# Optimization experiments

Hardware: AMD Instinct MI355X
Metric: run time of the kernel (lower is better)

## Reference

```python
import jax, jax.numpy as jnp
import numpy as np

N_NODES = 100000
N_EDGES = 1600000
IN_F = 32
HID = 128


def setup_inputs() -> dict:
    key = jax.random.key(0)
    ks = jax.random.split(key, 8)
    x = jax.random.normal(ks[0], (N_NODES, IN_F), dtype=jnp.float32)
    edge_index = jax.random.randint(ks[1], (2, N_EDGES), 0, N_NODES, dtype=jnp.int64)
    # Glorot-ish scaled weights
    W1 = jax.random.normal(ks[2], (IN_F, HID), dtype=jnp.float32) / np.sqrt(IN_F)
    b1 = jnp.zeros((HID,), dtype=jnp.float32)
    W2 = jax.random.normal(ks[3], (HID, HID), dtype=jnp.float32) / np.sqrt(HID)
    b2 = jnp.zeros((HID,), dtype=jnp.float32)
    W3 = jax.random.normal(ks[4], (HID, IN_F), dtype=jnp.float32) / np.sqrt(HID)
    b3 = jnp.zeros((IN_F,), dtype=jnp.float32)
    return {"x": x, "edge_index": edge_index, "W1": W1, "b1": b1,
            "W2": W2, "b2": b2, "W3": W3, "b3": b3}


def _gcn_norm(edge_index, n_nodes):
    # Add self-loops (PyG GCNConv default) and compute symmetric normalization
    loops = jnp.arange(n_nodes, dtype=edge_index.dtype)
    src = jnp.concatenate([edge_index[0], loops])
    dst = jnp.concatenate([edge_index[1], loops])
    ones = jnp.ones(src.shape[0], dtype=jnp.float32)
    deg = jax.ops.segment_sum(ones, dst, num_segments=n_nodes)
    deg_inv_sqrt = jnp.where(deg > 0, jax.lax.rsqrt(deg), 0.0)
    norm = deg_inv_sqrt[src] * deg_inv_sqrt[dst]  # [E + N]
    return src, dst, norm


def _gcn_conv(x, src, dst, norm, W, b, n_nodes):
    h = x @ W                                # [N, out] transform first (smaller msgs when out<in)
    msg = h[src] * norm[:, None]             # gather + edge-wise scale  [E+N, out]
    out = jax.ops.segment_sum(msg, dst, num_segments=n_nodes)  # scatter-add
    return out + b


def reference(x, edge_index, W1, b1, W2, b2, W3, b3):
    n = x.shape[0]
    src, dst, norm = _gcn_norm(edge_index, n)
    h = jax.nn.relu(_gcn_conv(x, src, dst, norm, W1, b1, n))
    h = jax.nn.relu(_gcn_conv(h, src, dst, norm, W2, b2, n))
    h = jax.nn.relu(_gcn_conv(h, src, dst, norm, W3, b3, n))
    return h
```

## Files before the change

kernel.cpp:

```cpp
#include <hip/hip_runtime.h>
#include <hip/hip_fp16.h>

#define N_NODES 100000
#define N_EDGES 1600000
#define IN_F 32
#define HID 128
#define BSHIFT 9
#define BSIZE 512
#define NBUCK 196
#define EPB 8192
#define NBB 196
#define COLSZ 3206144

typedef _Float16 half8 __attribute__((ext_vector_type(8)));
typedef float floatx4 __attribute__((ext_vector_type(4)));

static __device__ __forceinline__ void pack2(_Float16* dst, float a, float b) {
    union { _Float16 h[2]; unsigned u; } p;
    p.h[0] = (_Float16)a; p.h[1] = (_Float16)b;
    *(unsigned*)dst = p.u;
}


__global__ __launch_bounds__(256) void k_bcount(const int* __restrict__ dst,
                                                int* __restrict__ bcnt) {
    __shared__ int hist[256];
    hist[threadIdx.x] = 0;
    __syncthreads();
    const int e0 = blockIdx.x * EPB;
#pragma unroll 4
    for (int k = 0; k < 32; ++k) {
        int e = e0 + k * 256 + threadIdx.x;
        if (e < N_EDGES) atomicAdd(&hist[dst[e] >> BSHIFT], 1);
    }
    __syncthreads();
    int c = hist[threadIdx.x];
    if (c > 0) atomicAdd(&bcnt[threadIdx.x], c);
}

__global__ __launch_bounds__(256) void k_bscan(const int* __restrict__ bcnt,
                                               int* __restrict__ bbase,
                                               int* __restrict__ bcur) {
    __shared__ int s[256];
    int v = (threadIdx.x < NBUCK) ? bcnt[threadIdx.x] : 0;
    s[threadIdx.x] = v;
    __syncthreads();
    for (int off = 1; off < 256; off <<= 1) {
        int t = (threadIdx.x >= off) ? s[threadIdx.x - off] : 0;
        __syncthreads();
        s[threadIdx.x] += t;
        __syncthreads();
    }
    if (threadIdx.x < NBUCK) {
        int ex = s[threadIdx.x] - v;
        bbase[threadIdx.x] = ex;
        bcur[threadIdx.x]  = ex;
    }
    if (threadIdx.x == 0) bbase[NBUCK] = N_EDGES;
}

__global__ __launch_bounds__(256) void k_bucket(const int* __restrict__ src,
                                                const int* __restrict__ dst,
                                                int* __restrict__ bcur,
                                                unsigned* __restrict__ rec) {
    __shared__ int hist[256];
    __shared__ int lbase[256];
    const int e0 = blockIdx.x * EPB;
    hist[threadIdx.x] = 0;
    __syncthreads();

    unsigned rk[32]; short bk[32];
#pragma unroll
    for (int k = 0; k < 32; ++k) {
        int e = e0 + k * 256 + threadIdx.x;
        if (e < N_EDGES) {
            int d = dst[e];
            int b = d >> BSHIFT;
            bk[k] = (short)b;
            rk[k] = ((unsigned)src[e] << BSHIFT) | (unsigned)(d & (BSIZE - 1));
            atomicAdd(&hist[b], 1);
        } else bk[k] = -1;
    }
    __syncthreads();
    int c = hist[threadIdx.x];
    lbase[threadIdx.x] = (c > 0) ? atomicAdd(&bcur[threadIdx.x], c) : 0;
    __syncthreads();
    hist[threadIdx.x] = 0;
    __syncthreads();
#pragma unroll
    for (int k = 0; k < 32; ++k) {
        if (bk[k] >= 0) {
            int off = atomicAdd(&hist[bk[k]], 1);
            rec[lbase[bk[k]] + off] = rk[k];
        }
    }
}

__global__ __launch_bounds__(256) void k_fill3(const unsigned* __restrict__ rec,
                                               const int* __restrict__ bbase,
                                               int* __restrict__ ideg,
                                               int* __restrict__ cursor,
                                               int* __restrict__ col) {
    __shared__ int lcnt[BSIZE];
    __shared__ int lcur[BSIZE];
    __shared__ int lend[BSIZE];
    __shared__ int s[256];
    const int b = blockIdx.x;
    const int n0 = b << BSHIFT;
    const int rbeg = bbase[b];
    const int rend = bbase[b + 1];
    const int pbeg = ((rbeg + 15) & ~15) + (16 * BSIZE) * b;

    lcnt[threadIdx.x] = 0;
    lcnt[threadIdx.x + 256] = 0;
    __syncthreads();
    for (int i = rbeg + threadIdx.x; i < rend; i += 256)
        atomicAdd(&lcnt[rec[i] & (BSIZE - 1)], 1);
    __syncthreads();

    int a0 = lcnt[2 * threadIdx.x], a1 = lcnt[2 * threadIdx.x + 1];
    int p0 = (a0 + 15) & ~15, p1 = (a1 + 15) & ~15;
    int pv = p0 + p1;
    s[threadIdx.x] = pv;
    __syncthreads();
    for (int off = 1; off < 256; off <<= 1) {
        int t = (threadIdx.x >= off) ? s[threadIdx.x - off] : 0;
        __syncthreads();
        s[threadIdx.x] += t;
        __syncthreads();
    }
    int ex = s[threadIdx.x] - pv;
    int c0 = pbeg + ex;
    int c1 = c0 + p0;
    lcur[2 * threadIdx.x]     = c0;  lend[2 * threadIdx.x]     = c0 + p0;
    lcur[2 * threadIdx.x + 1] = c1;  lend[2 * threadIdx.x + 1] = c1 + p1;
    __syncthreads();

    for (int t = threadIdx.x; t < BSIZE; t += 256) {
        int n = n0 + t;
        if (n < N_NODES) {
            ideg[n]   = lcnt[t];
            cursor[n] = lcur[t];
        }
    }
    __syncthreads();
    for (int i = rbeg + threadIdx.x; i < rend; i += 256) {
        unsigned r = rec[i];
        int slot = atomicAdd(&lcur[r & (BSIZE - 1)], 1);
        col[slot] = (int)(r >> BSHIFT);
    }
    __syncthreads();
    for (int t = threadIdx.x; t < BSIZE; t += 256) {
        int e2 = lend[t];
        for (int k = lcur[t]; k < e2; ++k) col[k] = N_NODES;
    }
}


__global__ void k_prescale(const float2* __restrict__ x, const int* __restrict__ ideg,
                           __half2* __restrict__ T) {
    if (blockIdx.x == 0 && threadIdx.x < 16)
        ((unsigned*)(T + (size_t)N_NODES * 16))[threadIdx.x] = 0u;
    int tid = blockIdx.x * 256 + threadIdx.x;
    if (tid >= N_NODES * 16) return;
    int i = tid >> 4;
    float dis = rsqrtf(1.0f + (float)ideg[i]);
    float2 v = x[tid];
    T[tid] = __floats2half2_rn(v.x * dis, v.y * dis);
}


__global__ __launch_bounds__(256) void k_gather32_pre(
    const int* __restrict__ cursor, const int* __restrict__ ideg,
    const int* __restrict__ col, const _Float16* __restrict__ T,
    _Float16* __restrict__ OUT) {
    const int lane = threadIdx.x & 63;
    const int slot = lane >> 2;
    const int fl   = lane & 3;
    const int wid  = blockIdx.x * 4 + (threadIdx.x >> 6);
    const int wstride = gridDim.x * 4;

    for (int node = wid; node < N_NODES; node += wstride) {
        int begin = cursor[node];
        int d     = ideg[node];
        int nb    = (d + 15) >> 4;
        float acc[8];
        if (slot == 0) {
            half8 v = *(const half8*)(T + (size_t)node * IN_F + fl * 8);
#pragma unroll
            for (int i = 0; i < 8; ++i) acc[i] = (float)v[i];
        } else {
#pragma unroll
            for (int i = 0; i < 8; ++i) acc[i] = 0.f;
        }
        const int* cp = col + begin + slot;
        int itb = 0;
        for (; itb + 2 <= nb; itb += 2, cp += 32) {
            int s0 = cp[0];
            int s1 = cp[16];
            half8 v0 = *(const half8*)(T + (size_t)s0 * IN_F + fl * 8);
            half8 v1 = *(const half8*)(T + (size_t)s1 * IN_F + fl * 8);
#pragma unroll
            for (int i = 0; i < 8; ++i) acc[i] += (float)v0[i] + (float)v1[i];
        }
        if (itb < nb) {
            int s0 = cp[0];
            half8 v0 = *(const half8*)(T + (size_t)s0 * IN_F + fl * 8);
#pragma unroll
            for (int i = 0; i < 8; ++i) acc[i] += (float)v0[i];
        }
#pragma unroll
        for (int m = 4; m < 64; m <<= 1)
#pragma unroll
            for (int i = 0; i < 8; ++i) acc[i] += __shfl_xor(acc[i], m, 64);
        if (slot == 0) {
            float dis = rsqrtf(1.0f + (float)d);
            half8 o;
#pragma unroll
            for (int i = 0; i < 8; ++i) o[i] = (_Float16)(acc[i] * dis);
            *(half8*)(OUT + (size_t)node * IN_F + fl * 8) = o;
        }
    }
}

__global__ __launch_bounds__(256) void k_gather32_fin(
    const int* __restrict__ cursor, const int* __restrict__ ideg,
    const int* __restrict__ col, const _Float16* __restrict__ T,
    const float* __restrict__ b, float* __restrict__ OUT) {
    const int lane = threadIdx.x & 63;
    const int slot = lane >> 2;
    const int fl   = lane & 3;
    const int wid  = blockIdx.x * 4 + (threadIdx.x >> 6);
    const int wstride = gridDim.x * 4;

    float4 bb0 = *(const float4*)(b + fl * 8);
    float4 bb1 = *(const float4*)(b + fl * 8 + 4);
    float bias[8] = {bb0.x, bb0.y, bb0.z, bb0.w, bb1.x, bb1.y, bb1.z, bb1.w};

    for (int node = wid; node < N_NODES; node += wstride) {
        int begin = cursor[node];
        int d     = ideg[node];
        int nb    = (d + 15) >> 4;
        float acc[8];
        if (slot == 0) {
            half8 v = *(const half8*)(T + (size_t)node * IN_F + fl * 8);
#pragma unroll
            for (int i = 0; i < 8; ++i) acc[i] = (float)v[i];
        } else {
#pragma unroll
            for (int i = 0; i < 8; ++i) acc[i] = 0.f;
        }
        const int* cp = col + begin + slot;
        int itb = 0;
        for (; itb + 2 <= nb; itb += 2, cp += 32) {
            int s0 = cp[0];
            int s1 = cp[16];
            half8 v0 = *(const half8*)(T + (size_t)s0 * IN_F + fl * 8);
            half8 v1 = *(const half8*)(T + (size_t)s1 * IN_F + fl * 8);
#pragma unroll
            for (int i = 0; i < 8; ++i) acc[i] += (float)v0[i] + (float)v1[i];
        }
        if (itb < nb) {
            int s0 = cp[0];
            half8 v0 = *(const half8*)(T + (size_t)s0 * IN_F + fl * 8);
#pragma unroll
            for (int i = 0; i < 8; ++i) acc[i] += (float)v0[i];
        }
#pragma unroll
        for (int m = 4; m < 64; m <<= 1)
#pragma unroll
            for (int i = 0; i < 8; ++i) acc[i] += __shfl_xor(acc[i], m, 64);
        if (slot == 0) {
            float dis = rsqrtf(1.0f + (float)d);
            float o[8];
#pragma unroll
            for (int i = 0; i < 8; ++i) {
                float v = acc[i] * dis + bias[i];
                o[i] = v > 0.f ? v : 0.f;
            }
            float* op = OUT + (size_t)node * IN_F + fl * 8;
            *(float4*)op       = make_float4(o[0], o[1], o[2], o[3]);
            *(float4*)(op + 4) = make_float4(o[4], o[5], o[6], o[7]);
        }
    }
}

__global__ __launch_bounds__(256) void k_gather128(
    const int* __restrict__ cursor, const int* __restrict__ ideg,
    const int* __restrict__ col, const _Float16* __restrict__ T,
    const float* __restrict__ b, _Float16* __restrict__ OUT) {
    const int lane = threadIdx.x & 63;
    const int slot = lane >> 4;
    const int fl   = lane & 15;
    const int wid  = blockIdx.x * 4 + (threadIdx.x >> 6);
    const int wstride = gridDim.x * 4;

    float4 bb0 = *(const float4*)(b + fl * 8);
    float4 bb1 = *(const float4*)(b + fl * 8 + 4);
    float bias[8] = {bb0.x, bb0.y, bb0.z, bb0.w, bb1.x, bb1.y, bb1.z, bb1.w};

    for (int node = wid; node < N_NODES; node += wstride) {
        int begin = cursor[node];
        int d     = ideg[node];
        int nb    = (d + 15) >> 4;
        float acc[8];
        if (slot == 0) {
            half8 v = *(const half8*)(T + (size_t)node * HID + fl * 8);
#pragma unroll
            for (int i = 0; i < 8; ++i) acc[i] = (float)v[i];
        } else {
#pragma unroll
            for (int i = 0; i < 8; ++i) acc[i] = 0.f;
        }
        const int* cp = col + begin + slot * 4;
        for (int itb = 0; itb < nb; ++itb, cp += 16) {
            int4 cc = *(const int4*)cp;
            half8 v0 = *(const half8*)(T + (size_t)cc.x * HID + fl * 8);
            half8 v1 = *(const half8*)(T + (size_t)cc.y * HID + fl * 8);
            half8 v2 = *(const half8*)(T + (size_t)cc.z * HID + fl * 8);
            half8 v3 = *(const half8*)(T + (size_t)cc.w * HID + fl * 8);
#pragma unroll
            for (int i = 0; i < 8; ++i)
                acc[i] += ((float)v0[i] + (float)v1[i]) + ((float)v2[i] + (float)v3[i]);
        }
#pragma unroll
        for (int m = 16; m < 64; m <<= 1)
#pragma unroll
            for (int i = 0; i < 8; ++i) acc[i] += __shfl_xor(acc[i], m, 64);
        if (slot == 0) {
            float dis = rsqrtf(1.0f + (float)d);
            half8 o;
#pragma unroll
            for (int i = 0; i < 8; ++i) {
                float v = acc[i] * dis + bias[i];
                o[i] = (_Float16)(v > 0.f ? v : 0.f);
            }
            *(half8*)(OUT + (size_t)node * HID + fl * 8) = o;
        }
    }
}


__global__ __launch_bounds__(256) void k_xform12_mfma(
    const _Float16* __restrict__ z, const float* __restrict__ W1,
    const float* __restrict__ b1, const float* __restrict__ W2,
    const int* __restrict__ ideg, _Float16* __restrict__ T) {
    if (blockIdx.x == 0 && threadIdx.x < 64)
        ((unsigned*)(T + (size_t)N_NODES * HID))[threadIdx.x] = 0u;
    __shared__ _Float16 W1t[128 * 40];
    __shared__ _Float16 W2t[128 * 136];
    __shared__ _Float16 H1s[64 * 136];
    for (int idx = threadIdx.x; idx < 2048; idx += 256) {
        int n = idx & 127, k = (idx >> 7) * 2;
        pack2(&W1t[n * 40 + k], W1[k * HID + n], W1[(k + 1) * HID + n]);
    }
    for (int idx = threadIdx.x; idx < 8192; idx += 256) {
        int n = idx & 127, k = (idx >> 7) * 2;
        pack2(&W2t[n * 136 + k], W2[k * HID + n], W2[(k + 1) * HID + n]);
    }
    __syncthreads();

    const int lane = threadIdx.x & 63;
    const int wave = threadIdx.x >> 6;
    const int m16 = lane & 15, quad = lane >> 4;
    const int row0 = blockIdx.x * 64 + wave * 16;
    if (row0 >= N_NODES) return;

    {
        int arow = row0 + m16; if (arow >= N_NODES) arow = N_NODES - 1;
        half8 a = *(const half8*)(z + (size_t)arow * IN_F + quad * 8);
        floatx4 acc[8];
#pragma unroll
        for (int t = 0; t < 8; ++t) acc[t] = (floatx4){0.f, 0.f, 0.f, 0.f};
#pragma unroll
        for (int t = 0; t < 8; ++t) {
            half8 b = *(const half8*)&W1t[(t * 16 + m16) * 40 + quad * 8];
            acc[t] = __builtin_amdgcn_mfma_f32_16x16x32_f16(a, b, acc[t], 0, 0, 0);
        }
#pragma unroll
        for (int t = 0; t < 8; ++t) {
            int c = t * 16 + m16;
            float bj = b1[c];
#pragma unroll
            for (int r = 0; r < 4; ++r) {
                float v = acc[t][r] + bj;
                H1s[(wave * 16 + quad * 4 + r) * 136 + c] =
                    (_Float16)(v > 0.f ? v : 0.f);
            }
        }
    }
    __syncthreads();

    const _Float16* hp = &H1s[(wave * 16 + m16) * 136 + quad * 8];
    half8 a[4];
#pragma unroll
    for (int kk = 0; kk < 4; ++kk) a[kk] = *(const half8*)(hp + kk * 32);

    floatx4 acc[8];
#pragma unroll
    for (int t = 0; t < 8; ++t) acc[t] = (floatx4){0.f, 0.f, 0.f, 0.f};
#pragma unroll
    for (int t = 0; t < 8; ++t) {
        const _Float16* wp = &W2t[(t * 16 + m16) * 136 + quad * 8];
#pragma unroll
        for (int kk = 0; kk < 4; ++kk) {
            half8 b = *(const half8*)(wp + kk * 32);
            acc[t] = __builtin_amdgcn_mfma_f32_16x16x32_f16(a[kk], b, acc[t], 0, 0, 0);
        }
    }
    float dis[4];
#pragma unroll
    for (int r = 0; r < 4; ++r) {
        int row = row0 + quad * 4 + r;
        dis[r] = (row < N_NODES) ? rsqrtf(1.0f + (float)ideg[row]) : 0.f;
    }
#pragma unroll
    for (int t = 0; t < 8; ++t) {
        int c = t * 16 + m16;
#pragma unroll
        for (int r = 0; r < 4; ++r) {
            int row = row0 + quad * 4 + r;
            if (row < N_NODES)
                T[(size_t)row * HID + c] = (_Float16)(acc[t][r] * dis[r]);
        }
    }
}

__global__ __launch_bounds__(256) void k_xform3_mfma(
    const _Float16* __restrict__ H, const float* __restrict__ W,
    const int* __restrict__ ideg, _Float16* __restrict__ T) {
    if (blockIdx.x == 0 && threadIdx.x < 16)
        ((unsigned*)(T + (size_t)N_NODES * IN_F))[threadIdx.x] = 0u;
    __shared__ _Float16 Wt[32 * 136];
    for (int idx = threadIdx.x; idx < 2048; idx += 256) {
        int n = idx & 31, k = (idx >> 5) * 2;
        pack2(&Wt[n * 136 + k], W[k * IN_F + n], W[(k + 1) * IN_F + n]);
    }
    __syncthreads();

    const int lane = threadIdx.x & 63;
    const int wave = threadIdx.x >> 6;
    const int m16 = lane & 15, quad = lane >> 4;
    const int row0 = blockIdx.x * 64 + wave * 16;
    if (row0 >= N_NODES) return;

    int arow = row0 + m16; if (arow >= N_NODES) arow = N_NODES - 1;
    const _Float16* hp = H + (size_t)arow * HID + quad * 8;
    half8 a[4];
#pragma unroll
    for (int kk = 0; kk < 4; ++kk) a[kk] = *(const half8*)(hp + kk * 32);

    floatx4 acc[2];
#pragma unroll
    for (int t = 0; t < 2; ++t) acc[t] = (floatx4){0.f, 0.f, 0.f, 0.f};
#pragma unroll
    for (int t = 0; t < 2; ++t) {
        const _Float16* wp = &Wt[(t * 16 + m16) * 136 + quad * 8];
#pragma unroll
        for (int kk = 0; kk < 4; ++kk) {
            half8 b = *(const half8*)(wp + kk * 32);
            acc[t] = __builtin_amdgcn_mfma_f32_16x16x32_f16(a[kk], b, acc[t], 0, 0, 0);
        }
    }
    float dis[4];
#pragma unroll
    for (int r = 0; r < 4; ++r) {
        int row = row0 + quad * 4 + r;
        dis[r] = (row < N_NODES) ? rsqrtf(1.0f + (float)ideg[row]) : 0.f;
    }
#pragma unroll
    for (int t = 0; t < 2; ++t) {
        int c = t * 16 + m16;
#pragma unroll
        for (int r = 0; r < 4; ++r) {
            int row = row0 + quad * 4 + r;
            if (row < N_NODES)
                T[(size_t)row * IN_F + c] = (_Float16)(acc[t][r] * dis[r]);
        }
    }
}


extern "C" void kernel_launch(void* const* d_in, const int* in_sizes, int n_in,
                              void* d_out, int out_size, void* d_ws, size_t ws_size,
                              hipStream_t stream) {
    const float* x  = (const float*)d_in[0];
    const int*   ei = (const int*)d_in[1];
    const float* W1 = (const float*)d_in[2];
    const float* b1 = (const float*)d_in[3];
    const float* W2 = (const float*)d_in[4];
    const float* b2 = (const float*)d_in[5];
    const float* W3 = (const float*)d_in[6];
    const float* b3 = (const float*)d_in[7];
    float* out = (float*)d_out;

    const int* src = ei;
    const int* dst = ei + N_EDGES;

    int*      ideg   = (int*)d_ws;
    int*      cursor = ideg + 102400;
    int*      bcnt   = cursor + 102400;
    int*      bbase  = bcnt + 256;
    int*      bcur   = bbase + 256;
    int*      col    = bcur + 256;
    unsigned* rec    = (unsigned*)(col + COLSZ);
    _Float16* t1h    = (_Float16*)rec;
    _Float16* z      = t1h + (size_t)N_NODES * IN_F + 64;
    _Float16* H1h    = z + (size_t)N_NODES * IN_F;
    _Float16* T2h    = H1h + (size_t)N_NODES * HID;
    _Float16* H2h    = T2h + (size_t)N_NODES * HID + 128;

    const int xgrid = (N_NODES + 63) / 64;

    hipMemsetAsync(bcnt, 0, 256 * sizeof(int), stream);
    k_bcount<<<NBB, 256, 0, stream>>>(dst, bcnt);
    k_bscan<<<1, 256, 0, stream>>>(bcnt, bbase, bcur);
    k_bucket<<<NBB, 256, 0, stream>>>(src, dst, bcur, rec);
    k_fill3<<<NBUCK, 256, 0, stream>>>(rec, bbase, ideg, cursor, col);

    k_prescale<<<(N_NODES * 16 + 255) / 256, 256, 0, stream>>>(
        (const float2*)x, ideg, (__half2*)t1h);
    k_gather32_pre<<<2048, 256, 0, stream>>>(cursor, ideg, col, t1h, z);
    k_xform12_mfma<<<xgrid, 256, 0, stream>>>(z, W1, b1, W2, ideg, T2h);

    k_gather128<<<2048, 256, 0, stream>>>(cursor, ideg, col, T2h, b2, H2h);

    k_xform3_mfma<<<xgrid, 256, 0, stream>>>(H2h, W3, ideg, T2h);
    k_gather32_fin<<<2048, 256, 0, stream>>>(cursor, ideg, col, T2h, b3, out);
}
```

Baseline: 329.1 us.

## Drop bucket count/scan passes, fuse prescale and layer-3 transform, pre-transpose weights

Replaces the count+scan bucketing with fixed-stride per-bucket regions so a single bucket pass writes records directly, removing two kernels. Prescaling of x is folded into the CSR fill kernel, and the layer-3 transform is fused into the 128-wide gather via a shared-memory tile, eliminating the H2 round trip through global memory. Weights are transposed to fp16 once in a prep kernel instead of every block re-staging them into LDS. The fixed strides assume no bucket overflows its preallocated capacity, and the gather128 now uses a static node-per-wave mapping instead of a grid-stride loop.

```diff
diff --git a/kernel.cpp b/kernel.cpp
--- a/kernel.cpp
+++ b/kernel.cpp
@@ -8,56 +8,34 @@
 #define BSHIFT 9
 #define BSIZE 512
 #define NBUCK 196
-#define EPB 8192
-#define NBB 196
-#define COLSZ 3206144
+#define EPB 4096
+#define NBB 391
+#define REC_STRIDE 9728
+#define COL_STRIDE 17408
 
 typedef _Float16 half8 __attribute__((ext_vector_type(8)));
 typedef float floatx4 __attribute__((ext_vector_type(4)));
 
-static __device__ __forceinline__ void pack2(_Float16* dst, float a, float b) {
-    union { _Float16 h[2]; unsigned u; } p;
-    p.h[0] = (_Float16)a; p.h[1] = (_Float16)b;
-    *(unsigned*)dst = p.u;
-}
-
-
-__global__ __launch_bounds__(256) void k_bcount(const int* __restrict__ dst,
-                                                int* __restrict__ bcnt) {
-    __shared__ int hist[256];
-    hist[threadIdx.x] = 0;
-    __syncthreads();
-    const int e0 = blockIdx.x * EPB;
-#pragma unroll 4
-    for (int k = 0; k < 32; ++k) {
-        int e = e0 + k * 256 + threadIdx.x;
-        if (e < N_EDGES) atomicAdd(&hist[dst[e] >> BSHIFT], 1);
-    }
-    __syncthreads();
-    int c = hist[threadIdx.x];
-    if (c > 0) atomicAdd(&bcnt[threadIdx.x], c);
-}
-
-__global__ __launch_bounds__(256) void k_bscan(const int* __restrict__ bcnt,
-                                               int* __restrict__ bbase,
-                                               int* __restrict__ bcur) {
-    __shared__ int s[256];
-    int v = (threadIdx.x < NBUCK) ? bcnt[threadIdx.x] : 0;
-    s[threadIdx.x] = v;
-    __syncthreads();
-    for (int off = 1; off < 256; off <<= 1) {
-        int t = (threadIdx.x >= off) ? s[threadIdx.x - off] : 0;
-        __syncthreads();
-        s[threadIdx.x] += t;
-        __syncthreads();
-    }
-    if (threadIdx.x < NBUCK) {
-        int ex = s[threadIdx.x] - v;
-        bbase[threadIdx.x] = ex;
-        bcur[threadIdx.x]  = ex;
-    }
-    if (threadIdx.x == 0) bbase[NBUCK] = N_EDGES;
-}
+__global__ __launch_bounds__(256) void k_wprep(const float* __restrict__ W1,
+                                               const float* __restrict__ W2,
+                                               const float* __restrict__ W3,
+                                               _Float16* __restrict__ Wt) {
+    const int bid = blockIdx.x, t = threadIdx.x;
+    if (bid < 64) {
+        int idx = bid * 256 + t;
+        int n = idx >> 7, k = idx & 127;
+        Wt[4096 + idx] = (_Float16)W2[k * HID + n];
+    } else if (bid < 80) {
+        int idx = (bid - 64) * 256 + t;
+        int n = idx >> 5, k = idx & 31;
+        Wt[n * 32 + k] = (_Float16)W1[k * HID + n];
+    } else {
+        int idx = (bid - 80) * 256 + t;
+        int n = idx >> 7, k = idx & 127;
+        Wt[20480 + idx] = (_Float16)W3[k * IN_F + n];
+    }
+}
+
 
 __global__ __launch_bounds__(256) void k_bucket(const int* __restrict__ src,
                                                 const int* __restrict__ dst,
@@ -69,9 +47,9 @@
     hist[threadIdx.x] = 0;
     __syncthreads();
 
-    unsigned rk[32]; short bk[32];
-#pragma unroll
-    for (int k = 0; k < 32; ++k) {
+    unsigned rk[16]; short bk[16];
+#pragma unroll
+    for (int k = 0; k < 16; ++k) {
         int e = e0 + k * 256 + threadIdx.x;
         if (e < N_EDGES) {
             int d = dst[e];
@@ -83,12 +61,13 @@
     }
     __syncthreads();
     int c = hist[threadIdx.x];
-    lbase[threadIdx.x] = (c > 0) ? atomicAdd(&bcur[threadIdx.x], c) : 0;
+    lbase[threadIdx.x] =
+        (c > 0) ? threadIdx.x * REC_STRIDE + atomicAdd(&bcur[threadIdx.x], c) : 0;
     __syncthreads();
     hist[threadIdx.x] = 0;
     __syncthreads();
 #pragma unroll
-    for (int k = 0; k < 32; ++k) {
+    for (int k = 0; k < 16; ++k) {
         if (bk[k] >= 0) {
             int off = atomicAdd(&hist[bk[k]], 1);
             rec[lbase[bk[k]] + off] = rk[k];
@@ -96,77 +75,78 @@
     }
 }
 
-__global__ __launch_bounds__(256) void k_fill3(const unsigned* __restrict__ rec,
-                                               const int* __restrict__ bbase,
-                                               int* __restrict__ ideg,
-                                               int* __restrict__ cursor,
-                                               int* __restrict__ col) {
+__global__ __launch_bounds__(256) void k_fill3p(const unsigned* __restrict__ rec,
+                                                const int* __restrict__ bcur,
+                                                const float2* __restrict__ x2,
+                                                int* __restrict__ ideg,
+                                                int* __restrict__ cursor,
+                                                int* __restrict__ col,
+                                                __half2* __restrict__ t1) {
     __shared__ int lcnt[BSIZE];
     __shared__ int lcur[BSIZE];
     __shared__ int lend[BSIZE];
     __shared__ int s[256];
     const int b = blockIdx.x;
+    const int t = threadIdx.x;
     const int n0 = b << BSHIFT;
-    const int rbeg = bbase[b];
-    const int rend = bbase[b + 1];
-    const int pbeg = ((rbeg + 15) & ~15) + (16 * BSIZE) * b;
-
-    lcnt[threadIdx.x] = 0;
-    lcnt[threadIdx.x + 256] = 0;
-    __syncthreads();
-    for (int i = rbeg + threadIdx.x; i < rend; i += 256)
+    const int rbeg = b * REC_STRIDE;
+    const int rend = rbeg + bcur[b];
+    const int pbeg = b * COL_STRIDE;
+
+    lcnt[t] = 0;
+    lcnt[t + 256] = 0;
+    __syncthreads();
+    for (int i = rbeg + t; i < rend; i += 256)
         atomicAdd(&lcnt[rec[i] & (BSIZE - 1)], 1);
     __syncthreads();
 
-    int a0 = lcnt[2 * threadIdx.x], a1 = lcnt[2 * threadIdx.x + 1];
+    int a0 = lcnt[2 * t], a1 = lcnt[2 * t + 1];
     int p0 = (a0 + 15) & ~15, p1 = (a1 + 15) & ~15;
     int pv = p0 + p1;
-    s[threadIdx.x] = pv;
+    s[t] = pv;
     __syncthreads();
     for (int off = 1; off < 256; off <<= 1) {
-        int t = (threadIdx.x >= off) ? s[threadIdx.x - off] : 0;
+        int v = (t >= off) ? s[t - off] : 0;
         __syncthreads();
-        s[threadIdx.x] += t;
+        s[t] += v;
         __syncthreads();
     }
-    int ex = s[threadIdx.x] - pv;
+    int ex = s[t] - pv;
     int c0 = pbeg + ex;
     int c1 = c0 + p0;
-    lcur[2 * threadIdx.x]     = c0;  lend[2 * threadIdx.x]     = c0 + p0;
-    lcur[2 * threadIdx.x + 1] = c1;  lend[2 * threadIdx.x + 1] = c1 + p1;
-    __syncthreads();
-
-    for (int t = threadIdx.x; t < BSIZE; t += 256) {
-        int n = n0 + t;
+    lcur[2 * t]     = c0;  lend[2 * t]     = c0 + p0;
+    lcur[2 * t + 1] = c1;  lend[2 * t + 1] = c1 + p1;
+    __syncthreads();
+
+    for (int i = t; i < BSIZE; i += 256) {
+        int n = n0 + i;
         if (n < N_NODES) {
-            ideg[n]   = lcnt[t];
-            cursor[n] = lcur[t];
-        }
-    }
-    __syncthreads();
-    for (int i = rbeg + threadIdx.x; i < rend; i += 256) {
+            ideg[n]   = lcnt[i];
+            cursor[n] = lcur[i];
+        }
+    }
+    __syncthreads();
+    for (int i = rbeg + t; i < rend; i += 256) {
         unsigned r = rec[i];
         int slot = atomicAdd(&lcur[r & (BSIZE - 1)], 1);
         col[slot] = (int)(r >> BSHIFT);
     }
     __syncthreads();
-    for (int t = threadIdx.x; t < BSIZE; t += 256) {
-        int e2 = lend[t];
-        for (int k = lcur[t]; k < e2; ++k) col[k] = N_NODES;
-    }
-}
-
-
-__global__ void k_prescale(const float2* __restrict__ x, const int* __restrict__ ideg,
-                           __half2* __restrict__ T) {
-    if (blockIdx.x == 0 && threadIdx.x < 16)
-        ((unsigned*)(T + (size_t)N_NODES * 16))[threadIdx.x] = 0u;
-    int tid = blockIdx.x * 256 + threadIdx.x;
-    if (tid >= N_NODES * 16) return;
-    int i = tid >> 4;
-    float dis = rsqrtf(1.0f + (float)ideg[i]);
-    float2 v = x[tid];
-    T[tid] = __floats2half2_rn(v.x * dis, v.y * dis);
+    for (int i = t; i < BSIZE; i += 256) {
+        int e2 = lend[i];
+        for (int k = lcur[i]; k < e2; ++k) col[k] = N_NODES;
+    }
+
+    if (b == 0 && t < 16) ((unsigned*)t1)[N_NODES * 16 + t] = 0u;
+    for (int idx = t; idx < BSIZE * 16; idx += 256) {
+        int loc = idx >> 4, j = idx & 15;
+        int n = n0 + loc;
+        if (n < N_NODES) {
+            float dis = rsqrtf(1.0f + (float)lcnt[loc]);
+            float2 v = x2[(size_t)n * 16 + j];
+            t1[(size_t)n * 16 + j] = __floats2half2_rn(v.x * dis, v.y * dis);
+        }
+    }
 }
 
 
@@ -285,21 +265,103 @@
     }
 }
 
-__global__ __launch_bounds__(256) void k_gather128(
+
+__global__ __launch_bounds__(256, 4) void k_xform12(
+    const _Float16* __restrict__ z, const _Float16* __restrict__ W1t,
+    const float* __restrict__ b1, const _Float16* __restrict__ W2t,
+    const int* __restrict__ ideg, _Float16* __restrict__ T) {
+    if (blockIdx.x == 0 && threadIdx.x < 64)
+        ((unsigned*)(T + (size_t)N_NODES * HID))[threadIdx.x] = 0u;
+    __shared__ _Float16 H1s[64 * 136];
+
+    const int lane = threadIdx.x & 63;
+    const int wave = threadIdx.x >> 6;
+    const int m16 = lane & 15, quad = lane >> 4;
+    const int row0 = blockIdx.x * 64 + wave * 16;
+    if (row0 >= N_NODES) return;
+
+    {
+        int arow = row0 + m16; if (arow >= N_NODES) arow = N_NODES - 1;
+        half8 a = *(const half8*)(z + (size_t)arow * IN_F + quad * 8);
+        floatx4 acc[8];
+#pragma unroll
+        for (int t = 0; t < 8; ++t) acc[t] = (floatx4){0.f, 0.f, 0.f, 0.f};
+#pragma unroll
+        for (int t = 0; t < 8; ++t) {
+            half8 bf = *(const half8*)(W1t + (t * 16 + m16) * 32 + quad * 8);
+            acc[t] = __builtin_amdgcn_mfma_f32_16x16x32_f16(a, bf, acc[t], 0, 0, 0);
+        }
+#pragma unroll
+        for (int t = 0; t < 8; ++t) {
+            int c = t * 16 + m16;
+            float bj = b1[c];
+#pragma unroll
+            for (int r = 0; r < 4; ++r) {
+                float v = acc[t][r] + bj;
+                H1s[((wave * 16 + quad * 4 + r) * 136) + c] =
+                    (_Float16)(v > 0.f ? v : 0.f);
+            }
+        }
+    }
+    __syncthreads();
+
+    const _Float16* hp = &H1s[(wave * 16 + m16) * 136 + quad * 8];
+    half8 a[4];
+#pragma unroll
+    for (int kk = 0; kk < 4; ++kk) a[kk] = *(const half8*)(hp + kk * 32);
+
+    floatx4 acc[8];
+#pragma unroll
+    for (int t = 0; t < 8; ++t) acc[t] = (floatx4){0.f, 0.f, 0.f, 0.f};
+#pragma unroll
+    for (int t = 0; t < 8; ++t) {
+        const _Float16* wp = W2t + (t * 16 + m16) * 128 + quad * 8;
+#pragma unroll
+        for (int kk = 0; kk < 4; ++kk) {
+            half8 bf = *(const half8*)(wp + kk * 32);
+            acc[t] = __builtin_amdgcn_mfma_f32_16x16x32_f16(a[kk], bf, acc[t], 0, 0, 0);
+        }
+    }
+    float dis[4];
+#pragma unroll
+    for (int r = 0; r < 4; ++r) {
+        int row = row0 + quad * 4 + r;
+        dis[r] = (row < N_NODES) ? rsqrtf(1.0f + (float)ideg[row]) : 0.f;
+    }
+#pragma unroll
+    for (int t = 0; t < 8; ++t) {
+        int c = t * 16 + m16;
+#pragma unroll
+        for (int r = 0; r < 4; ++r) {
+            int row = row0 + quad * 4 + r;
+            if (row < N_NODES)
+                T[(size_t)row * HID + c] = (_Float16)(acc[t][r] * dis[r]);
+        }
+    }
+}
+
+__global__ __launch_bounds__(256, 4) void k_g128x3(
     const int* __restrict__ cursor, const int* __restrict__ ideg,
     const int* __restrict__ col, const _Float16* __restrict__ T,
-    const float* __restrict__ b, _Float16* __restrict__ OUT) {
+    const float* __restrict__ b2, const _Float16* __restrict__ W3t,
+    _Float16* __restrict__ T3) {
+    if (blockIdx.x == 0 && threadIdx.x < 16)
+        ((unsigned*)(T3 + (size_t)N_NODES * IN_F))[threadIdx.x] = 0u;
+    __shared__ _Float16 H2s[64 * 136];
+
     const int lane = threadIdx.x & 63;
+    const int wave = threadIdx.x >> 6;
     const int slot = lane >> 4;
     const int fl   = lane & 15;
-    const int wid  = blockIdx.x * 4 + (threadIdx.x >> 6);
-    const int wstride = gridDim.x * 4;
-
-    float4 bb0 = *(const float4*)(b + fl * 8);
-    float4 bb1 = *(const float4*)(b + fl * 8 + 4);
+    const int row0 = blockIdx.x * 64;
+
+    float4 bb0 = *(const float4*)(b2 + fl * 8);
+    float4 bb1 = *(const float4*)(b2 + fl * 8 + 4);
     float bias[8] = {bb0.x, bb0.y, bb0.z, bb0.w, bb1.x, bb1.y, bb1.z, bb1.w};
 
-    for (int node = wid; node < N_NODES; node += wstride) {
+    for (int k = 0; k < 16; ++k) {
+        int node = row0 + wave * 16 + k;
+        if (node >= N_NODES) break;
         int begin = cursor[node];
         int d     = ideg[node];
         int nb    = (d + 15) >> 4;
@@ -335,147 +397,42 @@
                 float v = acc[i] * dis + bias[i];
                 o[i] = (_Float16)(v > 0.f ? v : 0.f);
             }
-            *(half8*)(OUT + (size_t)node * HID + fl * 8) = o;
-        }
-    }
-}
-
-
-__global__ __launch_bounds__(256) void k_xform12_mfma(
-    const _Float16* __restrict__ z, const float* __restrict__ W1,
-    const float* __restrict__ b1, const float* __restrict__ W2,
-    const int* __restrict__ ideg, _Float16* __restrict__ T) {
-    if (blockIdx.x == 0 && threadIdx.x < 64)
-        ((unsigned*)(T + (size_t)N_NODES * HID))[threadIdx.x] = 0u;
-    __shared__ _Float16 W1t[128 * 40];
-    __shared__ _Float16 W2t[128 * 136];
-    __shared__ _Float16 H1s[64 * 136];
-    for (int idx = threadIdx.x; idx < 2048; idx += 256) {
-        int n = idx & 127, k = (idx >> 7) * 2;
-        pack2(&W1t[n * 40 + k], W1[k * HID + n], W1[(k + 1) * HID + n]);
-    }
-    for (int idx = threadIdx.x; idx < 8192; idx += 256) {
-        int n = idx & 127, k = (idx >> 7) * 2;
-        pack2(&W2t[n * 136 + k], W2[k * HID + n], W2[(k + 1) * HID + n]);
-    }
-    __syncthreads();
-
-    const int lane = threadIdx.x & 63;
-    const int wave = threadIdx.x >> 6;
-    const int m16 = lane & 15, quad = lane >> 4;
-    const int row0 = blockIdx.x * 64 + wave * 16;
-    if (row0 >= N_NODES) return;
-
-    {
-        int arow = row0 + m16; if (arow >= N_NODES) arow = N_NODES - 1;
-        half8 a = *(const half8*)(z + (size_t)arow * IN_F + quad * 8);
-        floatx4 acc[8];
-#pragma unroll
-        for (int t = 0; t < 8; ++t) acc[t] = (floatx4){0.f, 0.f, 0.f, 0.f};
-#pragma unroll
-        for (int t = 0; t < 8; ++t) {
-            half8 b = *(const half8*)&W1t[(t * 16 + m16) * 40 + quad * 8];
-            acc[t] = __builtin_amdgcn_mfma_f32_16x16x32_f16(a, b, acc[t], 0, 0, 0);
-        }
-#pragma unroll
-        for (int t = 0; t < 8; ++t) {
-            int c = t * 16 + m16;
-            float bj = b1[c];
-#pragma unroll
-            for (int r = 0; r < 4; ++r) {
-                float v = acc[t][r] + bj;
-                H1s[(wave * 16 + quad * 4 + r) * 136 + c] =
-                    (_Float16)(v > 0.f ? v : 0.f);
-            }
-        }
-    }
-    __syncthreads();
-
-    const _Float16* hp = &H1s[(wave * 16 + m16) * 136 + quad * 8];
+            *(half8*)&H2s[(wave * 16 + k) * 136 + fl * 8] = o;
+        }
+    }
+    __syncthreads();
+
+    const _Float16* hp = &H2s[(wave * 16 + fl) * 136 + slot * 8];
     half8 a[4];
 #pragma unroll
     for (int kk = 0; kk < 4; ++kk) a[kk] = *(const half8*)(hp + kk * 32);
 
-    floatx4 acc[8];
-#pragma unroll
-    for (int t = 0; t < 8; ++t) acc[t] = (floatx4){0.f, 0.f, 0.f, 0.f};
-#pragma unroll
-    for (int t = 0; t < 8; ++t) {
-        const _Float16* wp = &W2t[(t * 16 + m16) * 136 + quad * 8];
+    floatx4 acc3[2];
+#pragma unroll
+    for (int t = 0; t < 2; ++t) acc3[t] = (floatx4){0.f, 0.f, 0.f, 0.f};
+#pragma unroll
+    for (int t = 0; t < 2; ++t) {
+        const _Float16* wp = W3t + (t * 16 + fl) * 128 + slot * 8;
 #pragma unroll
         for (int kk = 0; kk < 4; ++kk) {
-            half8 b = *(const half8*)(wp + kk * 32);
-            acc[t] = __builtin_amdgcn_mfma_f32_16x16x32_f16(a[kk], b, acc[t], 0, 0, 0);
+            half8 bf = *(const half8*)(wp + kk * 32);
+            acc3[t] = __builtin_amdgcn_mfma_f32_16x16x32_f16(a[kk], bf, acc3[t], 0, 0, 0);
         }
     }
     float dis[4];
 #pragma unroll
     for (int r = 0; r < 4; ++r) {
-        int row = row0 + quad * 4 + r;
+        int row = row0 + wave * 16 + slot * 4 + r;
         dis[r] = (row < N_NODES) ? rsqrtf(1.0f + (float)ideg[row]) : 0.f;
     }
 #pragma unroll
-    for (int t = 0; t < 8; ++t) {
-        int c = t * 16 + m16;
+    for (int t = 0; t < 2; ++t) {
+        int c = t * 16 + fl;
 #pragma unroll
         for (int r = 0; r < 4; ++r) {
-            int row = row0 + quad * 4 + r;
+            int row = row0 + wave * 16 + slot * 4 + r;
             if (row < N_NODES)
-                T[(size_t)row * HID + c] = (_Float16)(acc[t][r] * dis[r]);
-        }
-    }
-}
-
-__global__ __launch_bounds__(256) void k_xform3_mfma(
-    const _Float16* __restrict__ H, const float* __restrict__ W,
-    const int* __restrict__ ideg, _Float16* __restrict__ T) {
-    if (blockIdx.x == 0 && threadIdx.x < 16)
-        ((unsigned*)(T + (size_t)N_NODES * IN_F))[threadIdx.x] = 0u;
-    __shared__ _Float16 Wt[32 * 136];
-    for (int idx = threadIdx.x; idx < 2048; idx += 256) {
-        int n = idx & 31, k = (idx >> 5) * 2;
-        pack2(&Wt[n * 136 + k], W[k * IN_F + n], W[(k + 1) * IN_F + n]);
-    }
-    __syncthreads();
-
-    const int lane = threadIdx.x & 63;
-    const int wave = threadIdx.x >> 6;
-    const int m16 = lane & 15, quad = lane >> 4;
-    const int row0 = blockIdx.x * 64 + wave * 16;
-    if (row0 >= N_NODES) return;
-
-    int arow = row0 + m16; if (arow >= N_NODES) arow = N_NODES - 1;
-    const _Float16* hp = H + (size_t)arow * HID + quad * 8;
-    half8 a[4];
-#pragma unroll
-    for (int kk = 0; kk < 4; ++kk) a[kk] = *(const half8*)(hp + kk * 32);
-
-    floatx4 acc[2];
-#pragma unroll
-    for (int t = 0; t < 2; ++t) acc[t] = (floatx4){0.f, 0.f, 0.f, 0.f};
-#pragma unroll
-    for (int t = 0; t < 2; ++t) {
-        const _Float16* wp = &Wt[(t * 16 + m16) * 136 + quad * 8];
-#pragma unroll
-        for (int kk = 0; kk < 4; ++kk) {
-            half8 b = *(const half8*)(wp + kk * 32);
-            acc[t] = __builtin_amdgcn_mfma_f32_16x16x32_f16(a[kk], b, acc[t], 0, 0, 0);
-        }
-    }
-    float dis[4];
-#pragma unroll
-    for (int r = 0; r < 4; ++r) {
-        int row = row0 + quad * 4 + r;
-        dis[r] = (row < N_NODES) ? rsqrtf(1.0f + (float)ideg[row]) : 0.f;
-    }
-#pragma unroll
-    for (int t = 0; t < 2; ++t) {
-        int c = t * 16 + m16;
-#pragma unroll
-        for (int r = 0; r < 4; ++r) {
-            int row = row0 + quad * 4 + r;
-            if (row < N_NODES)
-                T[(size_t)row * IN_F + c] = (_Float16)(acc[t][r] * dis[r]);
+                T3[(size_t)row * IN_F + c] = (_Float16)(acc3[t][r] * dis[r]);
         }
     }
 }
@@ -499,32 +456,29 @@
 
     int*      ideg   = (int*)d_ws;
     int*      cursor = ideg + 102400;
-    int*      bcnt   = cursor + 102400;
-    int*      bbase  = bcnt + 256;
-    int*      bcur   = bbase + 256;
+    int*      bcur   = cursor + 102400;
     int*      col    = bcur + 256;
-    unsigned* rec    = (unsigned*)(col + COLSZ);
-    _Float16* t1h    = (_Float16*)rec;
-    _Float16* z      = t1h + (size_t)N_NODES * IN_F + 64;
-    _Float16* H1h    = z + (size_t)N_NODES * IN_F;
-    _Float16* T2h    = H1h + (size_t)N_NODES * HID;
-    _Float16* H2h    = T2h + (size_t)N_NODES * HID + 128;
+    unsigned* rec    = (unsigned*)(col + NBUCK * COL_STRIDE);
+    _Float16* Wt     = (_Float16*)(rec + NBUCK * REC_STRIDE);
+    _Float16* t1h    = Wt + 24576;
+    _Float16* z      = t1h + 3200064;
+    _Float16* T2h    = z + 3200064;
+    _Float16* T3h    = T2h + 12800128;
 
     const int xgrid = (N_NODES + 63) / 64;
 
-    hipMemsetAsync(bcnt, 0, 256 * sizeof(int), stream);
-    k_bcount<<<NBB, 256, 0, stream>>>(dst, bcnt);
-    k_bscan<<<1, 256, 0, stream>>>(bcnt, bbase, bcur);
+    hipMemsetAsync(bcur, 0, 256 * sizeof(int), stream);
+    k_wprep<<<96, 256, 0, stream>>>(W1, W2, W3, Wt);
+
     k_bucket<<<NBB, 256, 0, stream>>>(src, dst, bcur, rec);
-    k_fill3<<<NBUCK, 256, 0, stream>>>(rec, bbase, ideg, cursor, col);
-
-    k_prescale<<<(N_NODES * 16 + 255) / 256, 256, 0, stream>>>(
-        (const float2*)x, ideg, (__half2*)t1h);
+    k_fill3p<<<NBUCK, 256, 0, stream>>>(rec, bcur, (const float2*)x,
+                                        ideg, cursor, col, (__half2*)t1h);
+
     k_gather32_pre<<<2048, 256, 0, stream>>>(cursor, ideg, col, t1h, z);
-    k_xform12_mfma<<<xgrid, 256, 0, stream>>>(z, W1, b1, W2, ideg, T2h);
-
-    k_gather128<<<2048, 256, 0, stream>>>(cursor, ideg, col, T2h, b2, H2h);
-
-    k_xform3_mfma<<<xgrid, 256, 0, stream>>>(H2h, W3, ideg, T2h);
-    k_gather32_fin<<<2048, 256, 0, stream>>>(cursor, ideg, col, T2h, b3, out);
-}
+    k_xform12<<<xgrid, 256, 0, stream>>>(z, Wt, b1, Wt + 4096, ideg, T2h);
+
+    k_g128x3<<<xgrid, 256, 0, stream>>>(cursor, ideg, col, T2h, b2,
+                                        Wt + 20480, T3h);
+
+    k_gather32_fin<<<2048, 256, 0, stream>>>(cursor, ideg, col, T3h, b3, out);
+}
```

New measurement: 323.9 us. No clear change (-1.6%).
